# Optimization experiments

Measured on AMD Instinct MI355X. Metric: run time of the kernel, lower is better.

## Reference

```python
import jax, jax.numpy as jnp
import numpy as np

B, S, H, D = 8, 1024, 1024, 64

def setup_inputs() -> dict:
    key = jax.random.key(0)
    ks = jax.random.split(key, 8)
    return {
        "query": jax.random.normal(ks[0], (B, S, H), jnp.float32),
        "key": jax.random.normal(ks[1], (B, S, H), jnp.float32),
        "value": jax.random.normal(ks[2], (B, S, H), jnp.float32),
        "Wq": jax.random.normal(ks[3], (H, D), jnp.float32) * 0.02,
        "bq": jnp.zeros((D,), jnp.float32),
        "Wk": jax.random.normal(ks[4], (H, D), jnp.float32) * 0.02,
        "bk": jnp.zeros((D,), jnp.float32),
        "Wv": jax.random.normal(ks[5], (H, D), jnp.float32) * 0.02,
        "bv": jnp.zeros((D,), jnp.float32),
        "k_bias_matrix": jax.random.normal(ks[6], (S, S, D), jnp.float32) * 0.02,
        "v_bias_matrix": jax.random.normal(ks[7], (S, S, D), jnp.float32) * 0.02,
        "mask": jnp.ones((B, S), jnp.int32),
    }

def reference(query, key, value, Wq, bq, Wk, bk, Wv, bv, k_bias_matrix, v_bias_matrix, mask):
    # Linear projections: [B,S,H] -> [B,S,D]
    q = query @ Wq + bq
    k = key @ Wk + bk
    v = value @ Wv + bv
    # Standard content score + Shaw relative-position key bias score
    attn_1 = jnp.einsum('bqd,bkd->bqk', q, k)
    attn_2 = jnp.einsum('bqd,qkd->bqk', q, k_bias_matrix)
    scores = (attn_1 + attn_2) / jnp.sqrt(jnp.float32(D))
    scores = jnp.where(mask[:, None, :] == 0, jnp.float32(-1e9), scores)
    w = jax.nn.softmax(scores, axis=-1)  # [B,S,S]
    values_1 = jnp.einsum('bqk,bkd->bqd', w, v)
    values_2 = jnp.einsum('bqk,qkd->bqd', w, v_bias_matrix)
    return values_1 + values_2
```

## Files before the change

kernel.cpp:

```cpp
#include <hip/hip_runtime.h>
#include <hip/hip_bf16.h>
#include <cstdint>
#include <cstddef>

#define NB 8
#define NS 1024
#define NH 1024
#define ND 64

typedef __attribute__((ext_vector_type(8))) short bf8_t;
typedef __attribute__((ext_vector_type(4))) float f32x4;
typedef __attribute__((ext_vector_type(4))) short short4v;

__device__ __forceinline__ short f2bfs(float x) {
    union { __hip_bfloat16 h; short s; } u;
    u.h = __float2bfloat16(x);
    return u.s;
}
__device__ __forceinline__ float bf2f(unsigned short h) {
    return __uint_as_float(((unsigned int)h) << 16);
}
__device__ __forceinline__ bf8_t pack_bf8(float4 a, float4 b) {
    bf8_t r;
    r[0] = f2bfs(a.x); r[1] = f2bfs(a.y); r[2] = f2bfs(a.z); r[3] = f2bfs(a.w);
    r[4] = f2bfs(b.x); r[5] = f2bfs(b.y); r[6] = f2bfs(b.z); r[7] = f2bfs(b.w);
    return r;
}

#define QP_OFF   0
#define KP_OFF   524288
#define VPT_OFF  1048576
#define S1_OFF   1572864
#define WT_OFF   9961472

__global__ __launch_bounds__(256, 8) void wcvt_kernel(
    const float* __restrict__ Wq, const float* __restrict__ Wk,
    const float* __restrict__ Wv, short* __restrict__ wt)
{
    const int p = blockIdx.y;
    const int n = blockIdx.x;
    const float* W = (p == 0) ? Wq : (p == 1) ? Wk : Wv;
    const int k0 = threadIdx.x * 4;
    short4v pk;
    #pragma unroll
    for (int i = 0; i < 4; ++i) pk[i] = f2bfs(W[(size_t)(k0 + i) * ND + n]);
    *(short4v*)&wt[((size_t)p * 64 + n) * 1024 + k0] = pk;
}

__global__ __launch_bounds__(256, 3) void proj_kernel(
    const float* __restrict__ qin, const float* __restrict__ kin, const float* __restrict__ vin,
    const short* __restrict__ wt,
    const float* __restrict__ bq, const float* __restrict__ bk, const float* __restrict__ bv,
    short* __restrict__ ws_s)
{
    __shared__ float red[2][16][68];

    const int p = blockIdx.y;
    const float* A    = (p == 0) ? qin : (p == 1) ? kin : vin;
    const float* bias = (p == 0) ? bq  : (p == 1) ? bk  : bv;

    const int t = threadIdx.x;
    const int wv = t >> 6, l = t & 63, lr = l & 15, lg = l >> 4;
    const int rt = wv >> 1, kh = wv & 1;
    const int rw = blockIdx.x * 32 + rt * 16;

    const short* wtp = wt + ((size_t)p * 64) * 1024 + kh * 512;
    const float* ab  = A + (size_t)(rw + lr) * NH + kh * 512;

    f32x4 acc[4];
    #pragma unroll
    for (int n = 0; n < 4; ++n) acc[n] = (f32x4){0.f, 0.f, 0.f, 0.f};

    #pragma unroll 2
    for (int ch = 0; ch < 4; ++ch) {
        #pragma unroll
        for (int s = 0; s < 4; ++s) {
            const int off = ch * 128 + s * 32 + lg * 8;
            bf8_t af = pack_bf8(*(const float4*)&ab[off], *(const float4*)&ab[off + 4]);
            #pragma unroll
            for (int n = 0; n < 4; ++n) {
                bf8_t bf = *(const bf8_t*)&wtp[(size_t)(n * 16 + lr) * 1024 + off];
                acc[n] = __builtin_amdgcn_mfma_f32_16x16x32_bf16(af, bf, acc[n], 0, 0, 0);
            }
        }
    }

    if (kh) {
        #pragma unroll
        for (int n = 0; n < 4; ++n)
            #pragma unroll
            for (int r = 0; r < 4; ++r)
                red[rt][lg * 4 + r][n * 16 + lr] = acc[n][r];
    }
    __syncthreads();
    if (!kh) {
        if (p < 2) {
            short* dst = ws_s + ((p == 0) ? QP_OFF : KP_OFF);
            const float sc = (p == 0) ? 0.125f : 1.0f;
            #pragma unroll
            for (int n = 0; n < 4; ++n) {
                const float bs = bias[n * 16 + lr];
                #pragma unroll
                for (int r = 0; r < 4; ++r) {
                    float v = acc[n][r] + red[rt][lg * 4 + r][n * 16 + lr] + bs;
                    dst[(size_t)(rw + lg * 4 + r) * ND + n * 16 + lr] = f2bfs(v * sc);
                }
            }
        } else {
            short* vpT = ws_s + VPT_OFF;
            const int b = rw >> 10;
            const int sbase = (rw & 1023) + lg * 4;
            #pragma unroll
            for (int n = 0; n < 4; ++n) {
                const float bs = bias[n * 16 + lr];
                short4v pk;
                #pragma unroll
                for (int r = 0; r < 4; ++r)
                    pk[r] = f2bfs(acc[n][r] + red[rt][lg * 4 + r][n * 16 + lr] + bs);
                *(short4v*)&vpT[((size_t)b * 64 + n * 16 + lr) * NS + sbase] = pk;
            }
        }
    }
}

__global__ __launch_bounds__(256, 4) void scores_c_kernel(
    const short* __restrict__ ws_s, short* __restrict__ s1)
{
    const short* qp = ws_s + QP_OFF;
    const short* kp = ws_s + KP_OFF;
    const int t = threadIdx.x;
    const int wv = t >> 6, l = t & 63, lr = l & 15, lg = l >> 4;
    const int q0 = blockIdx.y * 16;
    const int k0 = blockIdx.x * 64 + wv * 16;

    #pragma unroll
    for (int b = 0; b < 8; ++b) {
        const short* ap = &qp[((size_t)b * NS + q0 + lr) * ND + lg * 8];
        const short* bp = &kp[((size_t)b * NS + k0 + lr) * ND + lg * 8];
        bf8_t a0 = *(const bf8_t*)ap;
        bf8_t a1 = *(const bf8_t*)(ap + 32);
        bf8_t b0 = *(const bf8_t*)bp;
        bf8_t b1 = *(const bf8_t*)(bp + 32);
        f32x4 acc = {0.f, 0.f, 0.f, 0.f};
        acc = __builtin_amdgcn_mfma_f32_16x16x32_bf16(a0, b0, acc, 0, 0, 0);
        acc = __builtin_amdgcn_mfma_f32_16x16x32_bf16(a1, b1, acc, 0, 0, 0);
        #pragma unroll
        for (int r = 0; r < 4; ++r)
            s1[((size_t)b * NS + q0 + lg * 4 + r) * NS + k0 + lr] = f2bfs(acc[r]);
    }
}

__global__ __launch_bounds__(256, 4) void mega_kernel(
    const short* __restrict__ ws_s,
    short* __restrict__ s1,
    const float* __restrict__ kbias,
    const float* __restrict__ vbias,
    const int* __restrict__ mask,
    float* __restrict__ out)
{
    __shared__ __align__(16) short Sb[8][1032];
    __shared__ __align__(16) short Wt[8][1024];

    const short* qp = ws_s + QP_OFF;
    const int q = blockIdx.x, t = threadIdx.x;
    const int wv = t >> 6, l = t & 63, lr = l & 15, lg = l >> 4;

    {
        const bf8_t aq0 = *(const bf8_t*)&qp[((size_t)(lr & 7) * NS + q) * ND + lg * 8];
        const bf8_t aq1 = *(const bf8_t*)&qp[((size_t)(lr & 7) * NS + q) * ND + 32 + lg * 8];
        const float* kbq = kbias + (size_t)q * NS * ND;

        #pragma unroll
        for (int ith = 0; ith < 8; ++ith) {
            const int k0A = wv * 256 + (2 * ith) * 16;
            const int k0B = k0A + 16;
            const float* kA = &kbq[(size_t)(k0A + lr) * ND + lg * 8];
            const float* kB = &kbq[(size_t)(k0B + lr) * ND + lg * 8];
            float4 A0 = *(const float4*)kA;
            float4 A1 = *(const float4*)(kA + 4);
            float4 A2 = *(const float4*)(kA + 32);
            float4 A3 = *(const float4*)(kA + 36);
            float4 B0 = *(const float4*)kB;
            float4 B1 = *(const float4*)(kB + 4);
            float4 B2 = *(const float4*)(kB + 32);
            float4 B3 = *(const float4*)(kB + 36);

            f32x4 sA = {0.f, 0.f, 0.f, 0.f};
            sA = __builtin_amdgcn_mfma_f32_16x16x32_bf16(aq0, pack_bf8(A0, A1), sA, 0, 0, 0);
            sA = __builtin_amdgcn_mfma_f32_16x16x32_bf16(aq1, pack_bf8(A2, A3), sA, 0, 0, 0);
            f32x4 sB = {0.f, 0.f, 0.f, 0.f};
            sB = __builtin_amdgcn_mfma_f32_16x16x32_bf16(aq0, pack_bf8(B0, B1), sB, 0, 0, 0);
            sB = __builtin_amdgcn_mfma_f32_16x16x32_bf16(aq1, pack_bf8(B2, B3), sB, 0, 0, 0);

            if (lg < 2) {
                #pragma unroll
                for (int r = 0; r < 4; ++r) {
                    Sb[lg * 4 + r][k0A + lr] = f2bfs(sA[r]);
                    Sb[lg * 4 + r][k0B + lr] = f2bfs(sB[r]);
                }
            }
        }
    }
    __syncthreads();

    {
        const int b = t >> 5, idx = t & 31;
        const int kk = idx * 32;
        short* r1 = s1 + ((size_t)b * NS + q) * NS + kk;
        const int* mb = mask + b * NS + kk;
        const float LOG2E = 1.4426950408889634f;

        float x[32];
        float m = -3.0e38f;
        #pragma unroll
        for (int c = 0; c < 4; ++c) {
            uint4 a4 = *(const uint4*)&r1[8 * c];
            uint4 b4 = *(const uint4*)&Sb[b][kk + 8 * c];
            int4 m0 = *(const int4*)&mb[8 * c];
            int4 m1 = *(const int4*)&mb[8 * c + 4];
            const unsigned short* ap = (const unsigned short*)&a4;
            const unsigned short* bp = (const unsigned short*)&b4;
            const int* mp = (const int*)&m0;
            const int* mq = (const int*)&m1;
            #pragma unroll
            for (int j = 0; j < 8; ++j) {
                float v = bf2f(ap[j]) + bf2f(bp[j]);
                const int mvv = (j < 4) ? mp[j] : mq[j - 4];
                v = (mvv == 0) ? -1e9f : v;
                x[8 * c + j] = v;
                m = fmaxf(m, v);
            }
        }
        #pragma unroll
        for (int off = 1; off < 32; off <<= 1) m = fmaxf(m, __shfl_xor(m, off, 32));

        float lsum = 0.f;
        #pragma unroll
        for (int j = 0; j < 32; ++j) { x[j] = exp2f((x[j] - m) * LOG2E); lsum += x[j]; }
        #pragma unroll
        for (int off = 1; off < 32; off <<= 1) lsum += __shfl_xor(lsum, off, 32);
        const float il = 1.0f / fmaxf(lsum, 1e-30f);

        unsigned short wv16[32];
        #pragma unroll
        for (int j = 0; j < 32; ++j) wv16[j] = (unsigned short)f2bfs(x[j] * il);

        #pragma unroll
        for (int c = 0; c < 4; ++c) {
            *(uint4*)&r1[8 * c]         = *(const uint4*)&wv16[8 * c];
            *(uint4*)&Wt[b][kk + 8 * c] = *(const uint4*)&wv16[8 * c];
        }
    }
    __syncthreads();

    float* otile = (float*)&Sb[0][0];
    {
        const int kq = l >> 4, dq = l & 15;
        const int kw = wv * 256;
        const float* vbq = vbias + (size_t)q * NS * ND;

        float4 av[8];
        #pragma unroll
        for (int b = 0; b < 8; ++b) av[b] = make_float4(0.f, 0.f, 0.f, 0.f);

        short4v w4A[8];
        float4  vbA[4];
        {
            const int kb = kw + kq * 4;
            #pragma unroll
            for (int b = 0; b < 8; ++b) w4A[b] = *(const short4v*)&Wt[b][kb];
            #pragma unroll
            for (int j = 0; j < 4; ++j)
                vbA[j] = *(const float4*)&vbq[(size_t)(kb + j) * ND + 4 * dq];
        }

        #pragma unroll
        for (int i = 0; i < 16; ++i) {
            short4v w4B[8];
            float4  vbB[4];
            if (i < 15) {
                const int kb2 = kw + (i + 1) * 16 + kq * 4;
                #pragma unroll
                for (int b = 0; b < 8; ++b) w4B[b] = *(const short4v*)&Wt[b][kb2];
                #pragma unroll
                for (int j = 0; j < 4; ++j)
                    vbB[j] = *(const float4*)&vbq[(size_t)(kb2 + j) * ND + 4 * dq];
            }
            #pragma unroll
            for (int j = 0; j < 4; ++j) {
                #pragma unroll
                for (int b = 0; b < 8; ++b) {
                    const float wgt = bf2f((unsigned short)w4A[b][j]);
                    av[b].x += wgt * vbA[j].x; av[b].y += wgt * vbA[j].y;
                    av[b].z += wgt * vbA[j].z; av[b].w += wgt * vbA[j].w;
                }
            }
            if (i < 15) {
                #pragma unroll
                for (int b = 0; b < 8; ++b) w4A[b] = w4B[b];
                #pragma unroll
                for (int j = 0; j < 4; ++j) vbA[j] = vbB[j];
            }
        }

        #pragma unroll
        for (int b = 0; b < 8; ++b) {
            #pragma unroll
            for (int off = 16; off <= 32; off <<= 1) {
                av[b].x += __shfl_xor(av[b].x, off, 64);
                av[b].y += __shfl_xor(av[b].y, off, 64);
                av[b].z += __shfl_xor(av[b].z, off, 64);
                av[b].w += __shfl_xor(av[b].w, off, 64);
            }
        }
        if (l < 16) {
            #pragma unroll
            for (int b = 0; b < 8; ++b)
                *(float4*)&otile[((size_t)wv * 8 + b) * 64 + 4 * l] = av[b];
        }
    }
    __syncthreads();

    if (t < 128) {
        const int b = t >> 4, dd = (t & 15) * 4;
        float4 s = make_float4(0.f, 0.f, 0.f, 0.f);
        #pragma unroll
        for (int w4i = 0; w4i < 4; ++w4i) {
            float4 r = *(const float4*)&otile[((size_t)w4i * 8 + b) * 64 + dd];
            s.x += r.x; s.y += r.y; s.z += r.z; s.w += r.w;
        }
        *(float4*)&out[((size_t)b * NS + q) * ND + dd] = s;
    }
}

__global__ __launch_bounds__(256, 2) void v1_kernel(
    const short* __restrict__ ws_s, const short* __restrict__ w,
    float* __restrict__ out)
{
    const short* vpT = ws_s + VPT_OFF;
    const int t = threadIdx.x, wv = t >> 6, l = t & 63, lr = l & 15, lg = l >> 4;
    const int b = blockIdx.y;
    const int q0 = blockIdx.x * 16;

    f32x4 acc[4];
    #pragma unroll
    for (int j = 0; j < 4; ++j) acc[j] = (f32x4){0.f, 0.f, 0.f, 0.f};

    const short* arow = &w[((size_t)b * NS + q0 + lr) * NS + lg * 8];
    const short* brow = &vpT[((size_t)b * ND + wv * 16 + lr) * NS + lg * 8];
    #pragma unroll 8
    for (int ch = 0; ch < 32; ++ch) {
        bf8_t a  = *(const bf8_t*)(arow + ch * 32);
        bf8_t bb = *(const bf8_t*)(brow + ch * 32);
        acc[ch & 3] = __builtin_amdgcn_mfma_f32_16x16x32_bf16(a, bb, acc[ch & 3], 0, 0, 0);
    }
    f32x4 s;
    #pragma unroll
    for (int r = 0; r < 4; ++r) s[r] = acc[0][r] + acc[1][r] + acc[2][r] + acc[3][r];

    #pragma unroll
    for (int r = 0; r < 4; ++r) {
        float* op = &out[((size_t)b * NS + q0 + lg * 4 + r) * ND + wv * 16 + lr];
        *op = *op + s[r];
    }
}

extern "C" void kernel_launch(void* const* d_in, const int* in_sizes, int n_in,
                              void* d_out, int out_size, void* d_ws, size_t ws_size,
                              hipStream_t stream) {
    (void)in_sizes; (void)n_in; (void)out_size; (void)ws_size;
    const float* query = (const float*)d_in[0];
    const float* key   = (const float*)d_in[1];
    const float* value = (const float*)d_in[2];
    const float* Wq    = (const float*)d_in[3];
    const float* bq    = (const float*)d_in[4];
    const float* Wk    = (const float*)d_in[5];
    const float* bk    = (const float*)d_in[6];
    const float* Wv    = (const float*)d_in[7];
    const float* bv    = (const float*)d_in[8];
    const float* kbias = (const float*)d_in[9];
    const float* vbias = (const float*)d_in[10];
    const int*   mask  = (const int*)d_in[11];
    short* ws_s = (short*)d_ws;
    short* s1 = ws_s + S1_OFF;
    short* wt = ws_s + WT_OFF;
    float* outp = (float*)d_out;

    wcvt_kernel<<<dim3(64, 3), 256, 0, stream>>>(Wq, Wk, Wv, wt);
    proj_kernel<<<dim3(256, 3), 256, 0, stream>>>(query, key, value, wt, bq, bk, bv, ws_s);
    scores_c_kernel<<<dim3(16, 64), 256, 0, stream>>>(ws_s, s1);
    mega_kernel<<<1024, 256, 0, stream>>>(ws_s, s1, kbias, vbias, mask, outp);
    v1_kernel<<<dim3(64, 8), 256, 0, stream>>>(ws_s, s1, outp);
}
```

Before: 236.7 us.

## Reuse score LDS for softmax weights, shrink LDS, restructure v-bias accumulation loop

Stores the bf16 softmax weights back into the score buffer instead of a separate weight array, and gives the per-wave partial outputs their own small float tile. This cuts shared memory per block, which may let more blocks fit per CU. The k-bias loop is partly unrolled (unroll 2) instead of fully, and the v-bias loop drops the manual double-buffered prefetch in favour of a plain loop that reads 8 rows per iteration with 16-byte LDS loads. Register pressure and LDS use should fall, at the cost of less explicit overlap between global loads and FMAs.

```diff
diff --git a/kernel.cpp b/kernel.cpp
--- a/kernel.cpp
+++ b/kernel.cpp
@@ -159,7 +159,7 @@
     float* __restrict__ out)
 {
     __shared__ __align__(16) short Sb[8][1032];
-    __shared__ __align__(16) short Wt[8][1024];
+    __shared__ __align__(16) float otile[4][8][64];
 
     const short* qp = ws_s + QP_OFF;
     const int q = blockIdx.x, t = threadIdx.x;
@@ -170,9 +170,9 @@
         const bf8_t aq1 = *(const bf8_t*)&qp[((size_t)(lr & 7) * NS + q) * ND + 32 + lg * 8];
         const float* kbq = kbias + (size_t)q * NS * ND;
 
-        #pragma unroll
+        #pragma unroll 2
         for (int ith = 0; ith < 8; ++ith) {
-            const int k0A = wv * 256 + (2 * ith) * 16;
+            const int k0A = wv * 256 + ith * 32;
             const int k0B = k0A + 16;
             const float* kA = &kbq[(size_t)(k0A + lr) * ND + lg * 8];
             const float* kB = &kbq[(size_t)(k0B + lr) * ND + lg * 8];
@@ -248,12 +248,11 @@
         #pragma unroll
         for (int c = 0; c < 4; ++c) {
             *(uint4*)&r1[8 * c]         = *(const uint4*)&wv16[8 * c];
-            *(uint4*)&Wt[b][kk + 8 * c] = *(const uint4*)&wv16[8 * c];
+            *(uint4*)&Sb[b][kk + 8 * c] = *(const uint4*)&wv16[8 * c];
         }
     }
     __syncthreads();
 
-    float* otile = (float*)&Sb[0][0];
     {
         const int kq = l >> 4, dq = l & 15;
         const int kw = wv * 256;
@@ -263,46 +262,25 @@
         #pragma unroll
         for (int b = 0; b < 8; ++b) av[b] = make_float4(0.f, 0.f, 0.f, 0.f);
 
-        short4v w4A[8];
-        float4  vbA[4];
-        {
-            const int kb = kw + kq * 4;
-            #pragma unroll
-            for (int b = 0; b < 8; ++b) w4A[b] = *(const short4v*)&Wt[b][kb];
-            #pragma unroll
-            for (int j = 0; j < 4; ++j)
-                vbA[j] = *(const float4*)&vbq[(size_t)(kb + j) * ND + 4 * dq];
-        }
-
-        #pragma unroll
-        for (int i = 0; i < 16; ++i) {
-            short4v w4B[8];
-            float4  vbB[4];
-            if (i < 15) {
-                const int kb2 = kw + (i + 1) * 16 + kq * 4;
-                #pragma unroll
-                for (int b = 0; b < 8; ++b) w4B[b] = *(const short4v*)&Wt[b][kb2];
-                #pragma unroll
-                for (int j = 0; j < 4; ++j)
-                    vbB[j] = *(const float4*)&vbq[(size_t)(kb2 + j) * ND + 4 * dq];
-            }
-            #pragma unroll
-            for (int j = 0; j < 4; ++j) {
+        for (int ii = 0; ii < 8; ++ii) {
+            const int kb = kw + ii * 32 + kq * 8;
+            float4 vb[8];
+            #pragma unroll
+            for (int j = 0; j < 8; ++j)
+                vb[j] = *(const float4*)&vbq[(size_t)(kb + j) * ND + 4 * dq];
+            bf8_t w8[8];
+            #pragma unroll
+            for (int b = 0; b < 8; ++b) w8[b] = *(const bf8_t*)&Sb[b][kb];
+            #pragma unroll
+            for (int j = 0; j < 8; ++j) {
                 #pragma unroll
                 for (int b = 0; b < 8; ++b) {
-                    const float wgt = bf2f((unsigned short)w4A[b][j]);
-                    av[b].x += wgt * vbA[j].x; av[b].y += wgt * vbA[j].y;
-                    av[b].z += wgt * vbA[j].z; av[b].w += wgt * vbA[j].w;
+                    const float wgt = bf2f((unsigned short)w8[b][j]);
+                    av[b].x += wgt * vb[j].x; av[b].y += wgt * vb[j].y;
+                    av[b].z += wgt * vb[j].z; av[b].w += wgt * vb[j].w;
                 }
             }
-            if (i < 15) {
-                #pragma unroll
-                for (int b = 0; b < 8; ++b) w4A[b] = w4B[b];
-                #pragma unroll
-                for (int j = 0; j < 4; ++j) vbA[j] = vbB[j];
-            }
-        }
-
+        }
         #pragma unroll
         for (int b = 0; b < 8; ++b) {
             #pragma unroll
@@ -316,7 +294,7 @@
         if (l < 16) {
             #pragma unroll
             for (int b = 0; b < 8; ++b)
-                *(float4*)&otile[((size_t)wv * 8 + b) * 64 + 4 * l] = av[b];
+                *(float4*)&otile[wv][b][4 * l] = av[b];
         }
     }
     __syncthreads();
@@ -326,7 +304,7 @@
         float4 s = make_float4(0.f, 0.f, 0.f, 0.f);
         #pragma unroll
         for (int w4i = 0; w4i < 4; ++w4i) {
-            float4 r = *(const float4*)&otile[((size_t)w4i * 8 + b) * 64 + dd];
+            float4 r = *(const float4*)&otile[w4i][b][dd];
             s.x += r.x; s.y += r.y; s.z += r.z; s.w += r.w;
         }
         *(float4*)&out[((size_t)b * NS + q) * ND + dd] = s;
```

New measurement: 192.9 us. 1.23x faster.
